# Kernel tuning notes

Measured on AMD Instinct MI355X. Metric: run time of the kernel, lower is better.

The kernel has to match this reference:

```python
import jax, jax.numpy as jnp
import numpy as np

EMBED_DIM = 768
NUM_HEADS = 12
HEAD_DIM = EMBED_DIM // NUM_HEADS


def setup_inputs() -> dict:
    key = jax.random.key(0)
    k_x, k_qkv, k_w, k_b = jax.random.split(key, 4)
    B, N, D = 1, 4096, EMBED_DIM
    scale = 1.0 / np.sqrt(D)
    x = jax.random.normal(k_x, (B, N, D), dtype=jnp.float32)
    # nn.Linear weights: stored as [out, in]; we apply x @ W.T
    w_qkv = jax.random.normal(k_qkv, (3 * D, D), dtype=jnp.float32) * scale
    w_out = jax.random.normal(k_w, (D, D), dtype=jnp.float32) * scale
    b_out = jax.random.normal(k_b, (D,), dtype=jnp.float32) * 0.01
    return {"x": x, "w_qkv": w_qkv, "w_out": w_out, "b_out": b_out}


def reference(x, w_qkv, w_out, b_out):
    B, N, D = x.shape
    H, Hd = NUM_HEADS, HEAD_DIM
    qkv = (x @ w_qkv.T).reshape(B, N, 3, H, Hd)
    q, k, v = qkv[:, :, 0], qkv[:, :, 1], qkv[:, :, 2]
    scores = jnp.einsum('bnhd,bmhd->bhnm', q, k) / jnp.sqrt(jnp.float32(Hd))
    attn = jax.nn.softmax(scores, axis=-1)
    out = jnp.einsum('bhnm,bmhd->bnhd', attn, v).reshape(B, N, D)
    return out @ w_out.T + b_out
```

## Files before the change

kernel.cpp:

```cpp
#include <hip/hip_runtime.h>


typedef __attribute__((ext_vector_type(8))) short short8;
typedef __attribute__((ext_vector_type(4))) float f32x4;

#define N_TOK 4096
#define NHEAD 12
#define DMODEL 768
#define QK_LD 1536

#if defined(__has_builtin)
#if __has_builtin(__builtin_amdgcn_exp2f)
#define EXP2F __builtin_amdgcn_exp2f
#else
#define EXP2F exp2f
#endif
#else
#define EXP2F exp2f
#endif

#if defined(__has_builtin)
#if __has_builtin(__builtin_amdgcn_perm)
#define PACK2BF(hi, lo) __builtin_amdgcn_perm((hi), (lo), 0x07060302u)
#else
#define PACK2BF(hi, lo) ((((hi)) & 0xffff0000u) | (((lo)) >> 16))
#endif
#else
#define PACK2BF(hi, lo) ((((hi)) & 0xffff0000u) | (((lo)) >> 16))
#endif

__device__ __forceinline__ ushort bf16bits(float x) {
  union { float f; unsigned u; } cv; cv.f = x;
  unsigned u = cv.u;
  u += 0x7fffu + ((u >> 16) & 1u);
  return (ushort)(u >> 16);
}
__device__ __forceinline__ float bf2f(ushort u) {
  return __uint_as_float(((unsigned)u) << 16);
}

__device__ __forceinline__ void async16(ushort* lds, const ushort* g) {
  __builtin_amdgcn_global_load_lds((const __attribute__((address_space(1))) unsigned int*)g,
                                   (__attribute__((address_space(3))) unsigned int*)lds,
                                   16, 0, 0);
}

__global__ void __launch_bounds__(256) cvt3(const float* __restrict__ x,
                                            const float* __restrict__ wq,
                                            const float* __restrict__ wo,
                                            ushort* __restrict__ xb,
                                            ushort* __restrict__ wqb,
                                            ushort* __restrict__ wob) {
  const int b = blockIdx.x, t = threadIdx.x;
  const float* src; ushort* dst; int i;
  if (b < 3072)      { src = x;  dst = xb;  i = b * 256 + t; }
  else if (b < 4800) { src = wq; dst = wqb; i = (b - 3072) * 256 + t; }
  else               { src = wo; dst = wob; i = (b - 4800) * 256 + t; }
  const float4 v = ((const float4*)src)[i];
  ushort4 o;
  o.x = bf16bits(v.x); o.y = bf16bits(v.y); o.z = bf16bits(v.z); o.w = bf16bits(v.w);
  ((ushort4*)dst)[i] = o;
}

#define GEMM_STAGE(Ms, Mp, MK)                                                 \
  do {                                                                         \
    _Pragma("unroll")                                                          \
    for (int i_ = 0; i_ < 4; i_++)                                             \
      async16(&Ms[(wave * 32 + i_ * 8) * 64],                                  \
              Mp + (size_t)(wave * 32 + i_ * 8 + lrow) * (MK) + lcol);         \
  } while (0)

#define GEMM_STAGE96(Ms, Mp, MK)                                               \
  do {                                                                         \
    _Pragma("unroll")                                                          \
    for (int i_ = 0; i_ < 3; i_++)                                             \
      async16(&Ms[(wave * 24 + i_ * 8) * 64],                                  \
              Mp + (size_t)(wave * 24 + i_ * 8 + lrow) * (MK) + lcol);         \
  } while (0)

#define GEMM_STAGE64(Ms, Mp, MK)                                               \
  do {                                                                         \
    _Pragma("unroll")                                                          \
    for (int i_ = 0; i_ < 2; i_++)                                             \
      async16(&Ms[(wave * 16 + i_ * 8) * 64],                                  \
              Mp + (size_t)(wave * 16 + i_ * 8 + lrow) * (MK) + lcol);         \
  } while (0)

__global__ void __launch_bounds__(256) gemm_qkv(const ushort* __restrict__ A,
                                                const ushort* __restrict__ B,
                                                ushort* __restrict__ qkb,
                                                ushort* __restrict__ vtg) {
  __shared__ __align__(16) ushort As[128 * 64];
  __shared__ __align__(16) ushort Bs[96 * 64];
  const int tid = threadIdx.x;
  const int wave = tid >> 6, lane = tid & 63, quad = lane >> 4, l16 = lane & 15;
  const int wm = wave & 1, wn = wave >> 1;
  const int lrow = lane >> 3, lcol = (lane & 7) * 8;
  const int m0 = blockIdx.y * 128, n0 = blockIdx.x * 96;
  const int K = DMODEL;

  f32x4 acc[4][3] = {};
  const ushort* Ap = A + (size_t)m0 * K;
  const ushort* Bp = B + (size_t)n0 * K;

  for (int k0 = 0; k0 < K; k0 += 64) {
    GEMM_STAGE(As, Ap + k0, K);
    GEMM_STAGE96(Bs, Bp + k0, K);
    __syncthreads();
#pragma unroll
    for (int ks = 0; ks < 2; ks++) {
      short8 af[4], bf[3];
#pragma unroll
      for (int i = 0; i < 4; i++)
        af[i] = *(const short8*)&As[(wm * 64 + i * 16 + l16) * 64 + ks * 32 + quad * 8];
#pragma unroll
      for (int i = 0; i < 3; i++)
        bf[i] = *(const short8*)&Bs[(wn * 48 + i * 16 + l16) * 64 + ks * 32 + quad * 8];
#pragma unroll
      for (int mi = 0; mi < 4; mi++)
#pragma unroll
        for (int ni = 0; ni < 3; ni++)
          acc[mi][ni] = __builtin_amdgcn_mfma_f32_16x16x32_bf16(af[mi], bf[ni], acc[mi][ni], 0, 0, 0);
    }
    __syncthreads();
  }

  if (n0 < QK_LD) {
    const float qsc = (n0 < 768) ? 0.18033688011112042f : 1.0f;
#pragma unroll
    for (int mi = 0; mi < 4; mi++)
#pragma unroll
      for (int ni = 0; ni < 3; ni++) {
        const int col = n0 + wn * 48 + ni * 16 + l16;
#pragma unroll
        for (int rr = 0; rr < 4; rr++) {
          const int row = m0 + wm * 64 + mi * 16 + quad * 4 + rr;
          qkb[(size_t)row * QK_LD + col] = bf16bits(acc[mi][ni][rr] * qsc);
        }
      }
  } else {
#pragma unroll
    for (int mi = 0; mi < 4; mi++)
#pragma unroll
      for (int ni = 0; ni < 3; ni++) {
        const int col = n0 + wn * 48 + ni * 16 + l16 - QK_LD;
        const int rowb = m0 + wm * 64 + mi * 16 + quad * 4;
        const unsigned u0 = (unsigned)bf16bits(acc[mi][ni][0]) |
                            ((unsigned)bf16bits(acc[mi][ni][1]) << 16);
        const unsigned u1 = (unsigned)bf16bits(acc[mi][ni][2]) |
                            ((unsigned)bf16bits(acc[mi][ni][3]) << 16);
        *(uint2*)&vtg[(size_t)col * N_TOK + rowb] = make_uint2(u0, u1);
      }
  }
}

__global__ void __launch_bounds__(256) gemm_out(const ushort* __restrict__ A,
                                                const ushort* __restrict__ B,
                                                float* __restrict__ Cf,
                                                const float* __restrict__ bias) {
  __shared__ __align__(16) ushort As[64 * 64];
  __shared__ __align__(16) ushort Bs[64 * 64];
  const int tid = threadIdx.x;
  const int wave = tid >> 6, lane = tid & 63, quad = lane >> 4, l16 = lane & 15;
  const int wm = wave & 1, wn = wave >> 1;
  const int lrow = lane >> 3, lcol = (lane & 7) * 8;
  const int m0 = blockIdx.y * 64, n0 = blockIdx.x * 64;
  const int K = DMODEL, Nn = DMODEL;

  f32x4 acc[2][2] = {};
  const ushort* Ap = A + (size_t)m0 * K;
  const ushort* Bp = B + (size_t)n0 * K;

  for (int k0 = 0; k0 < K; k0 += 64) {
    GEMM_STAGE64(As, Ap + k0, K);
    GEMM_STAGE64(Bs, Bp + k0, K);
    __syncthreads();
#pragma unroll
    for (int ks = 0; ks < 2; ks++) {
      short8 af[2], bf[2];
#pragma unroll
      for (int i = 0; i < 2; i++) {
        af[i] = *(const short8*)&As[(wm * 32 + i * 16 + l16) * 64 + ks * 32 + quad * 8];
        bf[i] = *(const short8*)&Bs[(wn * 32 + i * 16 + l16) * 64 + ks * 32 + quad * 8];
      }
#pragma unroll
      for (int mi = 0; mi < 2; mi++)
#pragma unroll
        for (int ni = 0; ni < 2; ni++)
          acc[mi][ni] = __builtin_amdgcn_mfma_f32_16x16x32_bf16(af[mi], bf[ni], acc[mi][ni], 0, 0, 0);
    }
    __syncthreads();
  }

#pragma unroll
  for (int mi = 0; mi < 2; mi++)
#pragma unroll
    for (int ni = 0; ni < 2; ni++) {
      const int col = n0 + wn * 32 + ni * 16 + l16;
#pragma unroll
      for (int rr = 0; rr < 4; rr++) {
        const int row = m0 + wm * 32 + mi * 16 + quad * 4 + rr;
        Cf[(size_t)row * Nn + col] = acc[mi][ni][rr] + bias[col];
      }
    }
}


#define ATTN_STAGE(bufi)                                                       \
  do {                                                                         \
    async16(&Ks[bufi][(wave * 16) * 64],     kp0);                             \
    async16(&Ks[bufi][(wave * 16 + 8) * 64], kp1);                             \
    async16(&Vs[bufi][(wave * 16) * 64],     vp0);                             \
    async16(&Vs[bufi][(wave * 16 + 8) * 64], vp1);                             \
    kp0 += (size_t)64 * QK_LD; kp1 += (size_t)64 * QK_LD;                      \
    vp0 += 64; vp1 += 64;                                                      \
  } while (0)

#define ATTN_TILE(KbP, VbP)                                                    \
  do {                                                                         \
    const ushort* Kb_ = (KbP);                                                 \
    const ushort* Vb_ = (VbP);                                                 \
    _Pragma("unroll")                                                          \
    for (int ks = 0; ks < 2; ks++) {                                           \
      union { unsigned u[4]; short8 v; } pfu0, pfu1;                           \
      _Pragma("unroll")                                                        \
      for (int h2 = 0; h2 < 2; h2++) {                                         \
        const int nt = 2 * ks + h2;                                            \
        const short8 kf0 = *(const short8*)&Kb_[(nt * 16 + l16) * 64 + u0];    \
        const short8 kf1 = *(const short8*)&Kb_[(nt * 16 + l16) * 64 + u1];    \
        f32x4 a0 = __builtin_amdgcn_mfma_f32_16x16x32_bf16(kf0, qf[0][0], z4, 0, 0, 0); \
        a0 = __builtin_amdgcn_mfma_f32_16x16x32_bf16(kf1, qf[0][1], a0, 0, 0, 0);       \
        f32x4 a1 = __builtin_amdgcn_mfma_f32_16x16x32_bf16(kf0, qf[1][0], z4, 0, 0, 0); \
        a1 = __builtin_amdgcn_mfma_f32_16x16x32_bf16(kf1, qf[1][1], a1, 0, 0, 0);       \
        {                                                                      \
          const float e0 = EXP2F(a0[0]);                                       \
          const float e1 = EXP2F(a0[1]);                                       \
          const float e2 = EXP2F(a0[2]);                                       \
          const float e3 = EXP2F(a0[3]);                                       \
          lsum[0] += (e0 + e1) + (e2 + e3);                                    \
          pfu0.u[2 * h2]     = PACK2BF(__float_as_uint(e1), __float_as_uint(e0)); \
          pfu0.u[2 * h2 + 1] = PACK2BF(__float_as_uint(e3), __float_as_uint(e2)); \
        }                                                                      \
        {                                                                      \
          const float e0 = EXP2F(a1[0]);                                       \
          const float e1 = EXP2F(a1[1]);                                       \
          const float e2 = EXP2F(a1[2]);                                       \
          const float e3 = EXP2F(a1[3]);                                       \
          lsum[1] += (e0 + e1) + (e2 + e3);                                    \
          pfu1.u[2 * h2]     = PACK2BF(__float_as_uint(e1), __float_as_uint(e0)); \
          pfu1.u[2 * h2 + 1] = PACK2BF(__float_as_uint(e3), __float_as_uint(e2)); \
        }                                                                      \
      }                                                                        \
      const short8 pf0 = pfu0.v, pf1 = pfu1.v;                                 \
      _Pragma("unroll")                                                        \
      for (int dt = 0; dt < 4; dt++) {                                         \
        const short8 vf = *(const short8*)&Vb_[(dt * 16 + l16) * 64 + (ks ? u1 : u0)]; \
        o[0][dt] = __builtin_amdgcn_mfma_f32_16x16x32_bf16(pf0, vf, o[0][dt], 0, 0, 0); \
        o[1][dt] = __builtin_amdgcn_mfma_f32_16x16x32_bf16(pf1, vf, o[1][dt], 0, 0, 0); \
      }                                                                        \
    }                                                                          \
  } while (0)

__global__ void __launch_bounds__(256, 4) attn_flash(const ushort* __restrict__ qk,
                                                     const ushort* __restrict__ vtg,
                                                     ushort* __restrict__ pob,
                                                     float* __restrict__ pl,
                                                     int ntiles, int nsl8) {
  __shared__ __align__(16) ushort Ks[2][64 * 64];
  __shared__ __align__(16) ushort Vs[2][64 * 64];

  const int b = blockIdx.x;
  const int s8 = b & 7;
  const int j = b >> 3;
  const int slice = s8 + 8 * (j % nsl8);
  const int qb = j / nsl8;
  const int h = slice % NHEAD;
  const int sp = slice / NHEAD;

  const int tid = threadIdx.x;
  const int wave = tid >> 6, lane = tid & 63, quad = lane >> 4, l16 = lane & 15;
  const int q0 = qb * 128 + wave * 32;

  short8 qf[2][2];
#pragma unroll
  for (int s = 0; s < 2; s++) {
    const ushort* qp = qk + (size_t)(q0 + s * 16 + l16) * QK_LD + h * 64 + quad * 8;
    qf[s][0] = *(const short8*)qp;
    qf[s][1] = *(const short8*)(qp + 32);
  }

  const int srow = wave * 16 + (lane >> 3);
  const int un = (((lane & 7) ^ (lane >> 3)) * 8);
  const int g0 = ((srow >> 5) << 5) + (((srow >> 2) & 3) << 3) +
                 (((srow >> 4) & 1) << 2) + (srow & 3);
  const int kt0 = sp * ntiles;
  const ushort* kp0 = qk + 768 + h * 64 + un + (size_t)(kt0 * 64 + g0) * QK_LD;
  const ushort* kp1 = kp0 + (size_t)16 * QK_LD;
  const ushort* vp0 = vtg + (size_t)(h * 64 + srow) * N_TOK + kt0 * 64 + un;
  const ushort* vp1 = vp0 + (size_t)8 * N_TOK;

  const int u0 = (quad ^ (l16 & 7)) * 8;
  const int u1 = u0 ^ 32;

  f32x4 o[2][4] = {};
  float lsum[2] = {};
  const f32x4 z4 = {};

  ATTN_STAGE(0);
  __syncthreads();

  for (int kt = 0; kt < ntiles; kt++) {
    if (kt + 1 < ntiles) ATTN_STAGE((kt + 1) & 1);
    ATTN_TILE(Ks[kt & 1], Vs[kt & 1]);
    __syncthreads();
  }

#pragma unroll
  for (int s = 0; s < 2; s++) {
    float lt = lsum[s];
    lt += __shfl_xor(lt, 16, 64);
    lt += __shfl_xor(lt, 32, 64);
#pragma unroll
    for (int rr = 0; rr < 4; rr++) {
      const float l = __shfl(lt, quad * 16 + quad * 4 + rr, 64);
      const float inv = 1.f / l;
      const int row = q0 + s * 16 + quad * 4 + rr;
      if (l16 == 0)
        pl[(size_t)(sp * NHEAD + h) * N_TOK + row] = l;
#pragma unroll
      for (int dt = 0; dt < 4; dt++)
        pob[((size_t)sp * N_TOK + row) * DMODEL + h * 64 + dt * 16 + l16] =
            bf16bits(o[s][dt][rr] * inv);
    }
  }
}

__global__ void __launch_bounds__(256) combine(const ushort* __restrict__ pob,
                                               const float* __restrict__ pl,
                                               ushort* __restrict__ aout, int S) {
  const int i = blockIdx.x * 256 + threadIdx.x;
  const int row = i / (DMODEL / 4);
  const int hd = (i % (DMODEL / 4)) * 4;
  const int h = hd >> 6;
  float lt = 0.f, a0 = 0.f, a1 = 0.f, a2 = 0.f, a3 = 0.f;
  for (int s = 0; s < S; s++) {
    const float l = pl[((size_t)s * NHEAD + h) * N_TOK + row];
    const ushort4 a = *(const ushort4*)&pob[((size_t)s * N_TOK + row) * DMODEL + hd];
    lt += l;
    a0 += l * bf2f(a.x); a1 += l * bf2f(a.y); a2 += l * bf2f(a.z); a3 += l * bf2f(a.w);
  }
  const float inv = 1.f / lt;
  ushort4 r;
  r.x = bf16bits(a0 * inv); r.y = bf16bits(a1 * inv);
  r.z = bf16bits(a2 * inv); r.w = bf16bits(a3 * inv);
  *(ushort4*)&aout[(size_t)row * DMODEL + hd] = r;
}

extern "C" void kernel_launch(void* const* d_in, const int* in_sizes, int n_in,
                              void* d_out, int out_size, void* d_ws, size_t ws_size,
                              hipStream_t stream) {
  const float* x     = (const float*)d_in[0];
  const float* w_qkv = (const float*)d_in[1];
  const float* w_out = (const float*)d_in[2];
  const float* b_out = (const float*)d_in[3];
  float* out = (float*)d_out;

  const size_t PO_UNIT = 6291456UL;
  const int S = (ws_size >= 4 * PO_UNIT + 20840448UL) ? 4 : 2;
  char* ws = (char*)d_ws;
  ushort* pob   = (ushort*)ws;
  ushort* xb    = (ushort*)ws;
  ushort* wqkvb = (ushort*)(ws + 6291456UL);
  ushort* qkb   = (ushort*)(ws + (size_t)S * PO_UNIT);
  ushort* vtg   = (ushort*)((char*)qkb + 12582912UL);
  ushort* woutb = (ushort*)((char*)vtg + 6291456UL);
  float*  pl    = (float*)((char*)woutb + 1179648UL);
  ushort* aoutb = qkb;

  cvt3<<<5376, 256, 0, stream>>>(x, w_qkv, w_out, xb, wqkvb, woutb);

  gemm_qkv<<<dim3(24, 32), 256, 0, stream>>>(xb, wqkvb, qkb, vtg);

  attn_flash<<<384 * S, 256, 0, stream>>>(qkb, vtg, pob, pl, 64 / S, (12 * S) / 8);

  combine<<<3072, 256, 0, stream>>>(pob, pl, aoutb, S);

  gemm_out<<<dim3(12, 64), 256, 0, stream>>>(aoutb, woutb, out, b_out);
}
```

Before: 188.7 us.

## Load K/V tiles directly from global into registers, dropping LDS staging

Replaces the LDS double-buffered K/V staging with per-wave direct global loads into registers. A register-level ping-pong prefetches the next K tile, and V fragments are read just before each PV MFMA group. This removes the LDS traffic and the per-tile __syncthreads. The cost is redundant global/L2 reads across the four waves of a block and higher register pressure, so the launch bound drops from 4 to 3 blocks per CU. The loop now steps two tiles at a time, which assumes ntiles is even.

```diff
diff --git a/kernel.cpp b/kernel.cpp
--- a/kernel.cpp
+++ b/kernel.cpp
@@ -206,69 +206,78 @@
 }
 
 
-#define ATTN_STAGE(bufi)                                                       \
-  do {                                                                         \
-    async16(&Ks[bufi][(wave * 16) * 64],     kp0);                             \
-    async16(&Ks[bufi][(wave * 16 + 8) * 64], kp1);                             \
-    async16(&Vs[bufi][(wave * 16) * 64],     vp0);                             \
-    async16(&Vs[bufi][(wave * 16 + 8) * 64], vp1);                             \
-    kp0 += (size_t)64 * QK_LD; kp1 += (size_t)64 * QK_LD;                      \
-    vp0 += 64; vp1 += 64;                                                      \
-  } while (0)
-
-#define ATTN_TILE(KbP, VbP)                                                    \
-  do {                                                                         \
-    const ushort* Kb_ = (KbP);                                                 \
-    const ushort* Vb_ = (VbP);                                                 \
-    _Pragma("unroll")                                                          \
-    for (int ks = 0; ks < 2; ks++) {                                           \
-      union { unsigned u[4]; short8 v; } pfu0, pfu1;                           \
-      _Pragma("unroll")                                                        \
-      for (int h2 = 0; h2 < 2; h2++) {                                         \
-        const int nt = 2 * ks + h2;                                            \
-        const short8 kf0 = *(const short8*)&Kb_[(nt * 16 + l16) * 64 + u0];    \
-        const short8 kf1 = *(const short8*)&Kb_[(nt * 16 + l16) * 64 + u1];    \
-        f32x4 a0 = __builtin_amdgcn_mfma_f32_16x16x32_bf16(kf0, qf[0][0], z4, 0, 0, 0); \
-        a0 = __builtin_amdgcn_mfma_f32_16x16x32_bf16(kf1, qf[0][1], a0, 0, 0, 0);       \
-        f32x4 a1 = __builtin_amdgcn_mfma_f32_16x16x32_bf16(kf0, qf[1][0], z4, 0, 0, 0); \
-        a1 = __builtin_amdgcn_mfma_f32_16x16x32_bf16(kf1, qf[1][1], a1, 0, 0, 0);       \
-        {                                                                      \
-          const float e0 = EXP2F(a0[0]);                                       \
-          const float e1 = EXP2F(a0[1]);                                       \
-          const float e2 = EXP2F(a0[2]);                                       \
-          const float e3 = EXP2F(a0[3]);                                       \
-          lsum[0] += (e0 + e1) + (e2 + e3);                                    \
-          pfu0.u[2 * h2]     = PACK2BF(__float_as_uint(e1), __float_as_uint(e0)); \
-          pfu0.u[2 * h2 + 1] = PACK2BF(__float_as_uint(e3), __float_as_uint(e2)); \
-        }                                                                      \
-        {                                                                      \
-          const float e0 = EXP2F(a1[0]);                                       \
-          const float e1 = EXP2F(a1[1]);                                       \
-          const float e2 = EXP2F(a1[2]);                                       \
-          const float e3 = EXP2F(a1[3]);                                       \
-          lsum[1] += (e0 + e1) + (e2 + e3);                                    \
-          pfu1.u[2 * h2]     = PACK2BF(__float_as_uint(e1), __float_as_uint(e0)); \
-          pfu1.u[2 * h2 + 1] = PACK2BF(__float_as_uint(e3), __float_as_uint(e2)); \
-        }                                                                      \
-      }                                                                        \
-      const short8 pf0 = pfu0.v, pf1 = pfu1.v;                                 \
-      _Pragma("unroll")                                                        \
-      for (int dt = 0; dt < 4; dt++) {                                         \
-        const short8 vf = *(const short8*)&Vb_[(dt * 16 + l16) * 64 + (ks ? u1 : u0)]; \
-        o[0][dt] = __builtin_amdgcn_mfma_f32_16x16x32_bf16(pf0, vf, o[0][dt], 0, 0, 0); \
-        o[1][dt] = __builtin_amdgcn_mfma_f32_16x16x32_bf16(pf1, vf, o[1][dt], 0, 0, 0); \
-      }                                                                        \
+#define LOADK(K0a, K0b, K1a, K1b, K2a, K2b, K3a, K3b, EXTRA)                   \
+  do {                                                                         \
+    K0a = *(const short8*)(kp0 + (EXTRA));                                     \
+    K0b = *(const short8*)(kp0 + (EXTRA) + 32);                                \
+    K1a = *(const short8*)(kp1 + (EXTRA));                                     \
+    K1b = *(const short8*)(kp1 + (EXTRA) + 32);                                \
+    K2a = *(const short8*)(kp2 + (EXTRA));                                     \
+    K2b = *(const short8*)(kp2 + (EXTRA) + 32);                                \
+    K3a = *(const short8*)(kp3 + (EXTRA));                                     \
+    K3b = *(const short8*)(kp3 + (EXTRA) + 32);                                \
+  } while (0)
+
+#define QKEXP(KF0, KF1, h2)                                                    \
+  do {                                                                         \
+    f32x4 a0 = __builtin_amdgcn_mfma_f32_16x16x32_bf16(KF0, qf[0][0], z4, 0, 0, 0); \
+    a0 = __builtin_amdgcn_mfma_f32_16x16x32_bf16(KF1, qf[0][1], a0, 0, 0, 0);  \
+    f32x4 a1 = __builtin_amdgcn_mfma_f32_16x16x32_bf16(KF0, qf[1][0], z4, 0, 0, 0); \
+    a1 = __builtin_amdgcn_mfma_f32_16x16x32_bf16(KF1, qf[1][1], a1, 0, 0, 0);  \
+    {                                                                          \
+      const float e0 = EXP2F(a0[0]), e1 = EXP2F(a0[1]);                        \
+      const float e2 = EXP2F(a0[2]), e3 = EXP2F(a0[3]);                        \
+      lsum[0] += (e0 + e1) + (e2 + e3);                                        \
+      pfu0.u[2 * (h2)]     = PACK2BF(__float_as_uint(e1), __float_as_uint(e0)); \
+      pfu0.u[2 * (h2) + 1] = PACK2BF(__float_as_uint(e3), __float_as_uint(e2)); \
     }                                                                          \
-  } while (0)
-
-__global__ void __launch_bounds__(256, 4) attn_flash(const ushort* __restrict__ qk,
+    {                                                                          \
+      const float e0 = EXP2F(a1[0]), e1 = EXP2F(a1[1]);                        \
+      const float e2 = EXP2F(a1[2]), e3 = EXP2F(a1[3]);                        \
+      lsum[1] += (e0 + e1) + (e2 + e3);                                        \
+      pfu1.u[2 * (h2)]     = PACK2BF(__float_as_uint(e1), __float_as_uint(e0)); \
+      pfu1.u[2 * (h2) + 1] = PACK2BF(__float_as_uint(e3), __float_as_uint(e2)); \
+    }                                                                          \
+  } while (0)
+
+#define PVQ(V0, V1, V2, V3)                                                    \
+  do {                                                                         \
+    const short8 pf0 = pfu0.v, pf1 = pfu1.v;                                   \
+    o[0][0] = __builtin_amdgcn_mfma_f32_16x16x32_bf16(pf0, V0, o[0][0], 0, 0, 0); \
+    o[1][0] = __builtin_amdgcn_mfma_f32_16x16x32_bf16(pf1, V0, o[1][0], 0, 0, 0); \
+    o[0][1] = __builtin_amdgcn_mfma_f32_16x16x32_bf16(pf0, V1, o[0][1], 0, 0, 0); \
+    o[1][1] = __builtin_amdgcn_mfma_f32_16x16x32_bf16(pf1, V1, o[1][1], 0, 0, 0); \
+    o[0][2] = __builtin_amdgcn_mfma_f32_16x16x32_bf16(pf0, V2, o[0][2], 0, 0, 0); \
+    o[1][2] = __builtin_amdgcn_mfma_f32_16x16x32_bf16(pf1, V2, o[1][2], 0, 0, 0); \
+    o[0][3] = __builtin_amdgcn_mfma_f32_16x16x32_bf16(pf0, V3, o[0][3], 0, 0, 0); \
+    o[1][3] = __builtin_amdgcn_mfma_f32_16x16x32_bf16(pf1, V3, o[1][3], 0, 0, 0); \
+  } while (0)
+
+#define ATTN_TILE_R(K0a, K0b, K1a, K1b, K2a, K2b, K3a, K3b, VP)                \
+  do {                                                                         \
+    const ushort* vp_ = (VP);                                                  \
+    const short8 v00 = *(const short8*)(vp_);                                  \
+    const short8 v01 = *(const short8*)(vp_ + (size_t)16 * N_TOK);             \
+    const short8 v02 = *(const short8*)(vp_ + (size_t)32 * N_TOK);             \
+    const short8 v03 = *(const short8*)(vp_ + (size_t)48 * N_TOK);             \
+    union { unsigned u[4]; short8 v; } pfu0, pfu1;                             \
+    QKEXP(K0a, K0b, 0);                                                        \
+    QKEXP(K1a, K1b, 1);                                                        \
+    PVQ(v00, v01, v02, v03);                                                   \
+    const short8 v10 = *(const short8*)(vp_ + 32);                             \
+    const short8 v11 = *(const short8*)(vp_ + (size_t)16 * N_TOK + 32);        \
+    const short8 v12 = *(const short8*)(vp_ + (size_t)32 * N_TOK + 32);        \
+    const short8 v13 = *(const short8*)(vp_ + (size_t)48 * N_TOK + 32);        \
+    QKEXP(K2a, K2b, 0);                                                        \
+    QKEXP(K3a, K3b, 1);                                                        \
+    PVQ(v10, v11, v12, v13);                                                   \
+  } while (0)
+
+__global__ void __launch_bounds__(256, 3) attn_flash(const ushort* __restrict__ qk,
                                                      const ushort* __restrict__ vtg,
                                                      ushort* __restrict__ pob,
                                                      float* __restrict__ pl,
                                                      int ntiles, int nsl8) {
-  __shared__ __align__(16) ushort Ks[2][64 * 64];
-  __shared__ __align__(16) ushort Vs[2][64 * 64];
-
   const int b = blockIdx.x;
   const int s8 = b & 7;
   const int j = b >> 3;
@@ -289,30 +298,33 @@
     qf[s][1] = *(const short8*)(qp + 32);
   }
 
-  const int srow = wave * 16 + (lane >> 3);
-  const int un = (((lane & 7) ^ (lane >> 3)) * 8);
-  const int g0 = ((srow >> 5) << 5) + (((srow >> 2) & 3) << 3) +
-                 (((srow >> 4) & 1) << 2) + (srow & 3);
+  const int tokperm = ((l16 >> 2) << 3) | (l16 & 3);
   const int kt0 = sp * ntiles;
-  const ushort* kp0 = qk + 768 + h * 64 + un + (size_t)(kt0 * 64 + g0) * QK_LD;
-  const ushort* kp1 = kp0 + (size_t)16 * QK_LD;
-  const ushort* vp0 = vtg + (size_t)(h * 64 + srow) * N_TOK + kt0 * 64 + un;
-  const ushort* vp1 = vp0 + (size_t)8 * N_TOK;
-
-  const int u0 = (quad ^ (l16 & 7)) * 8;
-  const int u1 = u0 ^ 32;
+  const size_t kstep = (size_t)64 * QK_LD;
+  const ushort* kp0 = qk + 768 + h * 64 + quad * 8
+                    + (size_t)(kt0 * 64 + tokperm) * QK_LD;
+  const ushort* kp1 = kp0 + (size_t)4 * QK_LD;
+  const ushort* kp2 = kp0 + (size_t)32 * QK_LD;
+  const ushort* kp3 = kp0 + (size_t)36 * QK_LD;
+  const ushort* vp = vtg + (size_t)(h * 64 + l16) * N_TOK + kt0 * 64 + quad * 8;
 
   f32x4 o[2][4] = {};
   float lsum[2] = {};
   const f32x4 z4 = {};
 
-  ATTN_STAGE(0);
-  __syncthreads();
-
-  for (int kt = 0; kt < ntiles; kt++) {
-    if (kt + 1 < ntiles) ATTN_STAGE((kt + 1) & 1);
-    ATTN_TILE(Ks[kt & 1], Vs[kt & 1]);
-    __syncthreads();
+  short8 kA0a, kA0b, kA1a, kA1b, kA2a, kA2b, kA3a, kA3b;
+  short8 kB0a, kB0b, kB1a, kB1b, kB2a, kB2b, kB3a, kB3b;
+
+  LOADK(kA0a, kA0b, kA1a, kA1b, kA2a, kA2b, kA3a, kA3b, 0);
+
+  for (int kt = 0; kt < ntiles; kt += 2) {
+    LOADK(kB0a, kB0b, kB1a, kB1b, kB2a, kB2b, kB3a, kB3b, kstep);
+    ATTN_TILE_R(kA0a, kA0b, kA1a, kA1b, kA2a, kA2b, kA3a, kA3b, vp);
+    kp0 += 2 * kstep; kp1 += 2 * kstep; kp2 += 2 * kstep; kp3 += 2 * kstep;
+    if (kt + 2 < ntiles)
+      LOADK(kA0a, kA0b, kA1a, kA1b, kA2a, kA2b, kA3a, kA3b, 0);
+    ATTN_TILE_R(kB0a, kB0b, kB1a, kB1b, kB2a, kB2b, kB3a, kB3b, vp + 64);
+    vp += 128;
   }
 
 #pragma unroll
```

New measurement: 308.6 us. 63.5% more time.
